# Kernel optimization log

Measured on AMD Instinct MI355X. Metric: run time of the kernel, lower is better.

The kernel has to match this reference:

```python
import jax, jax.numpy as jnp
import numpy as np
import math

RC = 5.0            # radial cutoff rc_rad
ZETA = [1, 2, 3, 4] # zeta list from configs['zeta']=4

def _angular_consts(z):
    # all (lx,ly,lz) with lx+ly+lz <= z (code generates n in range(z+1) and expands
    # each n into its non-negative integer triples)
    tri = []
    for lx in range(z + 1):
        for ly in range(z + 1 - lx):
            for lz in range(z + 1 - lx - ly):
                tri.append((lx, ly, lz))
    tri = np.array(tri, np.int32)
    n = tri.sum(1)
    # fact_norm = (n!/(lx!ly!lz!)) * (z!/((z-n)! n!)) = z! / ((z-n)! lx! ly! lz!)
    c = np.array([math.factorial(z) / (math.factorial(z - int(s)) * math.factorial(int(a)) * math.factorial(int(b)) * math.factorial(int(d)))
                  for (a, b, d), s in zip(tri, n)], np.float32)
    sign = ((-1.0) ** n).astype(np.float32)  # lambda=-1 channel: (1-cos)^z expansion
    return tri, c, sign

ANG = [_angular_consts(z) for z in ZETA]
silu = jax.nn.silu


def setup_inputs() -> dict:
    key = jax.random.key(0)
    ks = jax.random.split(key, 16)
    nat, npairs, Nrad, nzeta, emb, nelem = 2048, 65536, 8, 4, 4, 4
    feat = (Nrad + Nrad * 2 * nzeta) * emb  # 288
    L = 20.0
    pos = jax.random.uniform(ks[0], (nat, 3), jnp.float32) * L
    cell = L * jnp.eye(3, dtype=jnp.float32)
    i1 = jax.random.randint(ks[1], (npairs,), 0, nat, jnp.int32)
    i2 = jax.random.randint(ks[2], (npairs,), 0, nat, jnp.int32)
    shift = jnp.zeros((npairs, 3), jnp.int32)
    ids = jax.random.randint(ks[3], (nat,), 0, nelem, jnp.int32)
    onehot = jax.nn.one_hot(ids, nelem, dtype=jnp.float32)
    def W(k, i, o):
        return jax.random.normal(k, (i, o), jnp.float32) * 0.1
    return dict(
        positions=pos, cell=cell, species_onehot=onehot,
        sw1=W(ks[4], nelem, 64), sb1=jnp.zeros((64,), jnp.float32),
        sw2=W(ks[5], 64, emb), sb2=jnp.zeros((emb,), jnp.float32),
        rw1=W(ks[6], Nrad, 64), rb1=jnp.zeros((64,), jnp.float32),
        rw2=W(ks[7], 64, (nzeta + 1) * Nrad), rb2=jnp.zeros(((nzeta + 1) * Nrad,), jnp.float32),
        aw1=W(ks[8], feat, 256), ab1=jnp.zeros((256,), jnp.float32),
        aw2=W(ks[9], 256, 128), ab2=jnp.zeros((128,), jnp.float32),
        aw3=W(ks[10], 128, 1), ab3=jnp.zeros((1,), jnp.float32),
        first_atom_idx=i1, second_atom_idx=i2, shift_vectors=shift,
    )


def reference(positions, cell, species_onehot, sw1, sb1, sw2, sb2,
              rw1, rb1, rw2, rb2, aw1, ab1, aw2, ab2, aw3, ab3,
              first_atom_idx, second_atom_idx, shift_vectors):
    nat = positions.shape[0]
    Nrad = rw1.shape[0]
    nzeta = rw2.shape[1] // Nrad - 1
    # pair displacement vectors with PBC shifts
    rij = (positions[second_atom_idx] - positions[first_atom_idx]
           + shift_vectors.astype(jnp.float32) @ cell)            # [P,3]
    r = jnp.sqrt(jnp.sum(rij * rij, axis=-1) + 1e-12)             # [P]
    u = rij / r[:, None]                                          # unit vectors
    fc = jnp.where(r < RC, 0.5 * (jnp.cos(jnp.pi * r / RC) + 1.0), 0.0)
    # Gaussian radial basis -> learned radial functions (silu MLP, linear head)
    centers = jnp.linspace(0.0, RC, Nrad)
    w = RC / Nrad
    basis = jnp.exp(-((r[:, None] - centers) ** 2) / (2.0 * w * w)) * fc[:, None]
    rad = silu(basis @ rw1 + rb1) @ rw2 + rb2
    rad = rad.reshape(-1, nzeta + 1, Nrad) * fc[:, None, None]    # [P, nzeta+1, Nrad]
    # species encoder MLP -> per-atom embedding, gathered onto neighbor side
    semb = silu(species_onehot @ sw1 + sb1) @ sw2 + sb2           # [nat, emb]
    sp = semb[second_atom_idx]                                    # [P, emb]
    seg = lambda v: jax.ops.segment_sum(v, first_atom_idx, num_segments=nat)
    # two-body radial descriptor [nat, Nrad, emb]
    R = seg(rad[:, 0, :, None] * sp[:, None, :])
    feats = [R.reshape(nat, -1)]
    # three-body angular descriptors via multinomial (lx,ly,lz) expansion
    for zi in range(nzeta):
        tri, c, sign = ANG[zi]
        l = jnp.asarray(tri, jnp.float32)                         # [L,3]
        g = jnp.prod(u[:, None, :] ** l[None], axis=-1)           # [P,L] u^lx u^ly u^lz
        t = rad[:, 1 + zi, :, None, None] * g[:, None, :, None] * sp[:, None, None, :]
        G = seg(t)                                                # [nat,Nrad,L,emb]
        G2 = G * G
        Ap = jnp.einsum('inle,l->ine', G2, jnp.asarray(c))        # sum_jk f f (1+cos)^z
        Am = jnp.einsum('inle,l->ine', G2, jnp.asarray(c * sign)) # sum_jk f f (1-cos)^z
        feats += [Ap.reshape(nat, -1), Am.reshape(nat, -1)]
    F = jnp.concatenate(feats, axis=-1)                           # [nat, feature_size]
    h = silu(F @ aw1 + ab1)
    h = silu(h @ aw2 + ab2)
    e = h @ aw3 + ab3                                             # per-atom energies
    return jnp.sum(e)


if __name__ == '__main__':
    out = reference(**setup_inputs())
    print(out)
```

## Files before the change

### kernel.cpp

```cpp
#include <hip/hip_runtime.h>
#include <cmath>

#define NAT  2048
#define NP   65536
#define CAP  64
#define SCAP 8192
#define SSTR 120
#define PPB  256

__constant__ int GLX[70] = {0,
  0,0,0,1,
  0,0,0,0,0,0,1,1,1,2,
  0,0,0,0,0,0,0,0,0,0,1,1,1,1,1,1,2,2,2,3,
  0,0,0,0,0,0,0,0,0,0,0,0,0,0,0,1,1,1,1,1,1,1,1,1,1,2,2,2,2,2,2,3,3,3,4};
__constant__ int GLY[70] = {0,
  0,0,1,0,
  0,0,0,1,1,2,0,0,1,0,
  0,0,0,0,1,1,1,2,2,3,0,0,0,1,1,2,0,0,1,0,
  0,0,0,0,0,1,1,1,1,2,2,2,3,3,4,0,0,0,0,1,1,1,2,2,3,0,0,0,1,1,2,0,0,1,0};
__constant__ int GLZ[70] = {0,
  0,1,0,0,
  0,1,2,0,1,0,0,1,0,0,
  0,1,2,3,0,1,2,0,1,0,0,1,2,0,1,0,0,1,0,0,
  0,1,2,3,4,0,1,2,3,0,1,2,0,1,0,0,1,2,3,0,1,2,0,1,0,0,1,2,0,1,0,0,1,0,0};
__constant__ float C_ALL[69] = {
  1,1,1,1,
  1,2,1,2,2,1,2,2,2,1,
  1,3,3,1,3,6,3,3,3,1,3,6,3,6,6,3,3,3,3,1,
  1,4,6,4,1,4,12,12,4,6,12,6,4,4,1,4,12,12,4,12,24,12,12,12,4,6,12,6,12,12,6,4,4,4,1};
__constant__ float CS_ALL[69] = {
  1,-1,-1,-1,
  1,-2,1,-2,2,1,-2,2,2,1,
  1,-3,3,-1,-3,6,-3,3,-3,-1,-3,6,-3,6,-6,-3,3,-3,-3,-1,
  1,-4,6,-4,1,-4,12,-12,4,6,-12,6,-4,4,1,-4,12,-12,4,12,-24,12,-12,12,4,6,-12,6,-12,12,6,-4,4,4,1};
__constant__ int LTAB[4]    = {4,10,20,35};
__constant__ int CUMTAB[4]  = {0,4,14,34};
__constant__ int BASETAB[4] = {32,160,480,1120};

__device__ __forceinline__ float silu_f(float x){ return x / (1.0f + expf(-x)); }

__global__ void k_zero(int* __restrict__ p){
  const int idx = blockIdx.x*256 + threadIdx.x;
  if (idx < 2050) p[idx] = 0;
}

__global__ __launch_bounds__(256) void k_fstage(
    const float* __restrict__ pos, const float* __restrict__ cell,
    const float* __restrict__ oneh,
    const int* __restrict__ i1, const int* __restrict__ i2,
    const int* __restrict__ sv,
    const float* __restrict__ sw1, const float* __restrict__ sb1,
    const float* __restrict__ sw2, const float* __restrict__ sb2,
    const float* __restrict__ rw1, const float* __restrict__ rb1,
    const float* __restrict__ rw2, const float* __restrict__ rb2,
    int* __restrict__ cursor, int* __restrict__ nflat,
    int* __restrict__ ord_pid, int* __restrict__ ord_flat,
    float* __restrict__ staged)
{
  __shared__ float sembt[4][4];
  __shared__ int   spidL[PPB];
  __shared__ int   nsurvS, baseS;
  __shared__ float geo[8][5];
  __shared__ int   gspec[8];
  __shared__ float basis[8][8];
  __shared__ float hbuf[8][64];

  const int tid = threadIdx.x, lane = tid & 63, wid = tid >> 6;

  {
    float h = silu_f(sb1[lane] + sw1[wid*64 + lane]);
    const float4 w2 = ((const float4*)sw2)[lane];
    float q0=h*w2.x, q1=h*w2.y, q2=h*w2.z, q3=h*w2.w;
#pragma unroll
    for (int off=32; off>0; off>>=1){
      q0 += __shfl_xor(q0, off); q1 += __shfl_xor(q1, off);
      q2 += __shfl_xor(q2, off); q3 += __shfl_xor(q3, off);
    }
    if (lane < 4){
      float v = (lane==0) ? q0+sb2[0] : (lane==1) ? q1+sb2[1]
              : (lane==2) ? q2+sb2[2] : q3+sb2[3];
      sembt[wid][lane] = v;
    }
  }
  if (tid == 0) nsurvS = 0;
  __syncthreads();

  {
    const int p = blockIdx.x*PPB + tid;
    const int a = i1[p], b = i2[p];
    const float s0=(float)sv[p*3+0], s1=(float)sv[p*3+1], s2=(float)sv[p*3+2];
    const float rx = pos[b*3+0]-pos[a*3+0] + s0*cell[0]+s1*cell[3]+s2*cell[6];
    const float ry = pos[b*3+1]-pos[a*3+1] + s0*cell[1]+s1*cell[4]+s2*cell[7];
    const float rz = pos[b*3+2]-pos[a*3+2] + s0*cell[2]+s1*cell[5]+s2*cell[8];
    const float r = sqrtf(rx*rx+ry*ry+rz*rz + 1e-12f);
    if (r < 5.0f){
      int ls = atomicAdd(&nsurvS, 1);
      spidL[ls] = p;
    }
  }
  __syncthreads();
  const int ns = nsurvS;
  if (ns == 0) return;
  if (tid == 0) baseS = atomicAdd(nflat, ns);
  __syncthreads();
  const int fbase = baseS;

  if (tid < ns){
    const int p = spidL[tid];
    const int a = i1[p];
    const int fs = fbase + tid;
    int s = atomicAdd(&cursor[a], 1);
    if (s < CAP){ ord_pid[a*CAP+s] = p; ord_flat[a*CAP+s] = fs; }
  }
  __syncthreads();

  for (int j0=0; j0<ns; j0+=8){
    const int nj = (ns-j0 < 8) ? (ns-j0) : 8;
    if (tid < nj){
      const int p = spidL[j0+tid];
      const int a = i1[p], b = i2[p];
      const float s0=(float)sv[p*3+0], s1=(float)sv[p*3+1], s2=(float)sv[p*3+2];
      const float rx = pos[b*3+0]-pos[a*3+0] + s0*cell[0]+s1*cell[3]+s2*cell[6];
      const float ry = pos[b*3+1]-pos[a*3+1] + s0*cell[1]+s1*cell[4]+s2*cell[7];
      const float rz = pos[b*3+2]-pos[a*3+2] + s0*cell[2]+s1*cell[5]+s2*cell[8];
      const float r  = sqrtf(rx*rx+ry*ry+rz*rz + 1e-12f);
      const float inv= 1.0f/r;
      geo[tid][0]=r; geo[tid][1]=rx*inv; geo[tid][2]=ry*inv; geo[tid][3]=rz*inv;
      geo[tid][4]=0.5f*(cosf(0.6283185307179586f*r)+1.0f);
      const float o1=oneh[b*4+1], o2=oneh[b*4+2], o3=oneh[b*4+3];
      gspec[tid] = (int)(o1 + 2.0f*o2 + 3.0f*o3 + 0.5f);
    }
    __syncthreads();
    if (tid < nj*8){
      const int j=tid>>3, k=tid&7;
      const float d = geo[j][0] - (float)k*(5.0f/7.0f);
      basis[j][k] = expf(-d*d*1.28f)*geo[j][4];
    }
    __syncthreads();
    for (int idx=tid; idx<nj*64; idx+=256){
      const int j=idx>>6, o=idx&63;
      float h = rb1[o];
#pragma unroll
      for (int k=0;k<8;k++) h += basis[j][k]*rw1[k*64+o];
      hbuf[j][o] = silu_f(h);
    }
    __syncthreads();
    for (int idx=tid; idx<nj*40; idx+=256){
      const int j=idx/40, n=idx-j*40;
      float racc = rb2[n];
#pragma unroll 8
      for (int o=0;o<64;o++) racc += hbuf[j][o]*rw2[o*40+n];
      const int fs = fbase + j0 + j;
      if (fs < SCAP) staged[(size_t)fs*SSTR + n] = racc*geo[j][4];
    }
    for (int idx=tid; idx<nj*70; idx+=256){
      const int j=idx/70, l=idx-j*70;
      const float ux=geo[j][1], uy=geo[j][2], uz=geo[j][3];
      const int ex=GLX[l], ey=GLY[l], ez=GLZ[l];
      float g=1.f;
      for (int q=0;q<ex;q++) g*=ux;
      for (int q=0;q<ey;q++) g*=uy;
      for (int q=0;q<ez;q++) g*=uz;
      const int fs = fbase + j0 + j;
      if (fs < SCAP) staged[(size_t)fs*SSTR + 40 + l] = g;
    }
    if (tid < nj*4){
      const int j=tid>>2, e=tid&3;
      const int fs = fbase + j0 + j;
      if (fs < SCAP) staged[(size_t)fs*SSTR + 110 + e] = sembt[gspec[j]][e];
    }
    __syncthreads();
  }
}

__global__ __launch_bounds__(256) void k_feat(
    const int* __restrict__ cursor,
    const int* __restrict__ ord_pid, const int* __restrict__ ord_flat,
    const float* __restrict__ staged, float* __restrict__ Fout)
{
  const int atom = blockIdx.x, tid = threadIdx.x;
  __shared__ float G[2240];
  __shared__ float sdata[8][SSTR];
  __shared__ int opid[CAP];
  __shared__ int pslot[CAP];
  __shared__ int sflb[8];

  int cnt = cursor[atom]; if (cnt > CAP) cnt = CAP;
  if (tid < CAP) opid[tid] = (tid < cnt) ? ord_pid[atom*CAP + tid] : 0x7fffffff;
  __syncthreads();
  if (tid < cnt){
    int my = opid[tid]; int rk = 0;
    for (int j=0;j<cnt;j++) rk += (opid[j] < my);
    pslot[rk] = tid;
  }

  float acc[9];
  int ridx[9], gidx[9], eidx[9];
#pragma unroll
  for (int k=0;k<9;k++){
    acc[k]=0.f;
    int a = tid + (k<<8);
    int ri=0, gi=0, ei=0;
    if (a < 32){ ri = a>>2; gi = 0; ei = a&3; }
    else if (a < 2240){
      int b = a-32; int lb, nl, l, n;
      if (b < 128)      { lb=b;      ei=lb&3; nl=lb>>2; l=nl%4;  n=nl/4;  ri=8 +n; gi=1 +l; }
      else if (b < 448) { lb=b-128;  ei=lb&3; nl=lb>>2; l=nl%10; n=nl/10; ri=16+n; gi=5 +l; }
      else if (b < 1088){ lb=b-448;  ei=lb&3; nl=lb>>2; l=nl%20; n=nl/20; ri=24+n; gi=15+l; }
      else              { lb=b-1088; ei=lb&3; nl=lb>>2; l=nl%35; n=nl/35; ri=32+n; gi=35+l; }
    }
    ridx[k]=ri; gidx[k]=gi; eidx[k]=ei;
  }
  __syncthreads();

  for (int c0=0; c0<cnt; c0+=8){
    const int nc = (cnt-c0 < 8) ? (cnt-c0) : 8;
    if (tid < nc) sflb[tid] = ord_flat[atom*CAP + pslot[c0+tid]];
    __syncthreads();
    for (int idx=tid; idx<nc*SSTR; idx+=256){
      int jj = idx/SSTR, i = idx - jj*SSTR;
      int fsl = sflb[jj];
      sdata[jj][i] = (fsl < SCAP) ? staged[(size_t)fsl*SSTR + i] : 0.f;
    }
    __syncthreads();
    for (int jj=0;jj<nc;jj++){
      const float* sd = sdata[jj];
#pragma unroll
      for (int k=0;k<9;k++)
        acc[k] += sd[ridx[k]] * sd[40+gidx[k]] * sd[110+eidx[k]];
    }
    __syncthreads();
  }

#pragma unroll
  for (int k=0;k<9;k++){
    int a = tid + (k<<8);
    if (a < 2240) G[a] = acc[k];
  }
  __syncthreads();

  float* Fo = Fout + atom*288;
  if (tid < 32) Fo[tid] = G[tid];
  if (tid < 128){
    const int zi = tid>>5, n=(tid>>2)&7, e=tid&3;
    const int L = LTAB[zi], cb = CUMTAB[zi], bs = BASETAB[zi];
    float ap=0.f, am=0.f;
    for (int l=0;l<L;l++){
      float v  = G[bs + ((n*L + l)<<2) + e];
      float v2 = v*v;
      ap += C_ALL [cb+l]*v2;
      am += CS_ALL[cb+l]*v2;
    }
    Fo[32 + (zi<<6)      + (n<<2) + e] = ap;
    Fo[32 + (zi<<6) + 32 + (n<<2) + e] = am;
  }
}

__global__ __launch_bounds__(256) void k_mlpreg(
    const float* __restrict__ F,
    const float* __restrict__ aw1, const float* __restrict__ ab1,
    const float* __restrict__ aw2, const float* __restrict__ ab2,
    const float* __restrict__ aw3, const float* __restrict__ ab3,
    float* __restrict__ partials, int* __restrict__ done,
    float* __restrict__ out)
{
  __shared__ float Hs[8][256];
  __shared__ float es[8];
  __shared__ int   winner;
  const int tid = threadIdx.x;
  const int abase = blockIdx.x*8;

  {
    const int c = tid;
    float acc[8];
#pragma unroll
    for (int a=0;a<8;a++) acc[a]=0.f;
    const float* Fb = F + (size_t)abase*288;
    for (int i=0;i<288;i++){
      const float w = aw1[(size_t)i*256 + c];
#pragma unroll
      for (int a=0;a<8;a++)
        acc[a] += Fb[a*288 + i] * w;
    }
    const float b = ab1[c];
#pragma unroll
    for (int a=0;a<8;a++) Hs[a][c] = silu_f(acc[a] + b);
  }
  __syncthreads();

  {
    const int c2 = tid & 127, h = tid >> 7;
    float acc2[4] = {0.f,0.f,0.f,0.f};
    for (int i4=0; i4<256; i4+=4){
      const float w0 = aw2[(size_t)(i4+0)*128 + c2];
      const float w1 = aw2[(size_t)(i4+1)*128 + c2];
      const float w2 = aw2[(size_t)(i4+2)*128 + c2];
      const float w3 = aw2[(size_t)(i4+3)*128 + c2];
#pragma unroll
      for (int q=0;q<4;q++){
        const float4 h4 = *(const float4*)&Hs[h*4+q][i4];
        acc2[q] += h4.x*w0 + h4.y*w1 + h4.z*w2 + h4.w*w3;
      }
    }
    const float b  = ab2[c2];
    const float w3h = aw3[c2];
    float p = silu_f(acc2[0]+b)*w3h;
    float p1 = silu_f(acc2[1]+b)*w3h;
    float p2 = silu_f(acc2[2]+b)*w3h;
    float p3 = silu_f(acc2[3]+b)*w3h;
    __shared__ float part[4][4][2];
    const int wv = tid >> 6, lane = tid & 63;
    float s0=p, s1=p1, s2=p2, s3=p3;
#pragma unroll
    for (int off=32; off>0; off>>=1){
      s0 += __shfl_xor(s0, off); s1 += __shfl_xor(s1, off);
      s2 += __shfl_xor(s2, off); s3 += __shfl_xor(s3, off);
    }
    if (lane == 0){
      part[wv][0][0]=s0; part[wv][1][0]=s1; part[wv][2][0]=s2; part[wv][3][0]=s3;
    }
    __syncthreads();
    if (tid < 8){
      const int hh = tid >> 2, q = tid & 3;
      es[hh*4+q] = part[2*hh][q][0] + part[2*hh+1][q][0];
    }
  }
  __syncthreads();
  if (tid == 0){
    float bsum = es[0]+es[1]+es[2]+es[3]+es[4]+es[5]+es[6]+es[7] + 8.0f*ab3[0];
    __hip_atomic_store(&partials[blockIdx.x], bsum,
                       __ATOMIC_RELEASE, __HIP_MEMORY_SCOPE_AGENT);
    int old = __hip_atomic_fetch_add(done, 1, __ATOMIC_ACQ_REL,
                                     __HIP_MEMORY_SCOPE_AGENT);
    winner = (old == (NAT/8) - 1) ? 1 : 0;
  }
  __syncthreads();

  if (winner && tid < 64){
    float s = 0.f;
#pragma unroll
    for (int q=0;q<4;q++)
      s += __hip_atomic_load(&partials[tid*4+q],
                             __ATOMIC_ACQUIRE, __HIP_MEMORY_SCOPE_AGENT);
    for (int off=32; off>0; off>>=1) s += __shfl_xor(s, off);
    if (tid == 0) out[0] = s;
  }
}

extern "C" void kernel_launch(void* const* d_in, const int* in_sizes, int n_in,
                              void* d_out, int out_size, void* d_ws, size_t ws_size,
                              hipStream_t stream) {
  const float* pos  = (const float*)d_in[0];
  const float* cell = (const float*)d_in[1];
  const float* oneh = (const float*)d_in[2];
  const float* sw1  = (const float*)d_in[3];
  const float* sb1  = (const float*)d_in[4];
  const float* sw2  = (const float*)d_in[5];
  const float* sb2  = (const float*)d_in[6];
  const float* rw1  = (const float*)d_in[7];
  const float* rb1  = (const float*)d_in[8];
  const float* rw2  = (const float*)d_in[9];
  const float* rb2  = (const float*)d_in[10];
  const float* aw1  = (const float*)d_in[11];
  const float* ab1  = (const float*)d_in[12];
  const float* aw2  = (const float*)d_in[13];
  const float* ab2  = (const float*)d_in[14];
  const float* aw3  = (const float*)d_in[15];
  const float* ab3  = (const float*)d_in[16];
  const int*   i1   = (const int*)d_in[17];
  const int*   i2   = (const int*)d_in[18];
  const int*   sv   = (const int*)d_in[19];

  char* ws = (char*)d_ws;
  int*   cursor   = (int*)  (ws + 0);
  int*   nflat    = (int*)  (ws + 8192);
  int*   done     = (int*)  (ws + 8196);
  int*   ord_pid  = (int*)  (ws + 8448);
  int*   ord_flat = (int*)  (ws + 532736);
  float* staged   = (float*)(ws + 1057024);
  float* F        = (float*)(ws + 4989184);
  float* partials = (float*)(ws + 7348480);

  k_zero  <<<9,       256, 0, stream>>>(cursor);
  k_fstage<<<NP/PPB,  256, 0, stream>>>(pos, cell, oneh, i1, i2, sv,
                                        sw1, sb1, sw2, sb2,
                                        rw1, rb1, rw2, rb2,
                                        cursor, nflat, ord_pid, ord_flat, staged);
  k_feat  <<<NAT,     256, 0, stream>>>(cursor, ord_pid, ord_flat, staged, F);
  k_mlpreg<<<NAT/8,   256, 0, stream>>>(F, aw1, ab1, aw2, ab2, aw3, ab3,
                                        partials, done, (float*)d_out);
}
```

Measured before the change: 77.83 us.

## Split MLP reduction across 1024 threads and vectorize staged row gather

The MLP kernel now runs 1024 threads per block. The first layer's 288-long input dimension is split into four slices whose partial sums go to shared memory and are reduced there, and the second layer gives each thread one atom instead of four. This is meant to raise parallelism in the latency-bound MLP, which has only 256 blocks, at the cost of extra shared memory and a barrier. Separately, the per-pair staged row copy in k_feat now uses float4 loads, cutting the number of load instructions.

```diff
diff --git a/kernel.cpp b/kernel.cpp
--- a/kernel.cpp
+++ b/kernel.cpp
@@ -180,7 +180,7 @@
 {
   const int atom = blockIdx.x, tid = threadIdx.x;
   __shared__ float G[2240];
-  __shared__ float sdata[8][SSTR];
+  __shared__ __align__(16) float sdata[8][SSTR];
   __shared__ int opid[CAP];
   __shared__ int pslot[CAP];
   __shared__ int sflb[8];
@@ -217,10 +217,12 @@
     const int nc = (cnt-c0 < 8) ? (cnt-c0) : 8;
     if (tid < nc) sflb[tid] = ord_flat[atom*CAP + pslot[c0+tid]];
     __syncthreads();
-    for (int idx=tid; idx<nc*SSTR; idx+=256){
-      int jj = idx/SSTR, i = idx - jj*SSTR;
+    for (int idx=tid; idx<nc*30; idx+=256){
+      int jj = idx/30, q = idx - jj*30;
       int fsl = sflb[jj];
-      sdata[jj][i] = (fsl < SCAP) ? staged[(size_t)fsl*SSTR + i] : 0.f;
+      float4 v = make_float4(0.f,0.f,0.f,0.f);
+      if (fsl < SCAP) v = ((const float4*)(staged + (size_t)fsl*SSTR))[q];
+      ((float4*)sdata[jj])[q] = v;
     }
     __syncthreads();
     for (int jj=0;jj<nc;jj++){
@@ -256,7 +258,7 @@
   }
 }
 
-__global__ __launch_bounds__(256) void k_mlpreg(
+__global__ __launch_bounds__(1024) void k_mlp4(
     const float* __restrict__ F,
     const float* __restrict__ aw1, const float* __restrict__ ab1,
     const float* __restrict__ aw2, const float* __restrict__ ab2,
@@ -264,67 +266,63 @@
     float* __restrict__ partials, int* __restrict__ done,
     float* __restrict__ out)
 {
+  __shared__ float P1s[4][8][256];
   __shared__ float Hs[8][256];
+  __shared__ float part[16];
   __shared__ float es[8];
   __shared__ int   winner;
   const int tid = threadIdx.x;
   const int abase = blockIdx.x*8;
+  const float* Fb = F + (size_t)abase*288;
 
   {
-    const int c = tid;
+    const int q = tid >> 8, c = tid & 255;
+    const int i0 = q*72;
     float acc[8];
 #pragma unroll
     for (int a=0;a<8;a++) acc[a]=0.f;
-    const float* Fb = F + (size_t)abase*288;
-    for (int i=0;i<288;i++){
-      const float w = aw1[(size_t)i*256 + c];
+    for (int ib=0; ib<18; ++ib){
+      const int i = i0 + ib*4;
+      float4 f4[8];
+#pragma unroll
+      for (int a=0;a<8;a++) f4[a] = *(const float4*)&Fb[a*288 + i];
+      const float w0 = aw1[(size_t)(i+0)*256 + c];
+      const float w1 = aw1[(size_t)(i+1)*256 + c];
+      const float w2 = aw1[(size_t)(i+2)*256 + c];
+      const float w3 = aw1[(size_t)(i+3)*256 + c];
 #pragma unroll
       for (int a=0;a<8;a++)
-        acc[a] += Fb[a*288 + i] * w;
-    }
-    const float b = ab1[c];
-#pragma unroll
-    for (int a=0;a<8;a++) Hs[a][c] = silu_f(acc[a] + b);
+        acc[a] += f4[a].x*w0 + f4[a].y*w1 + f4[a].z*w2 + f4[a].w*w3;
+    }
+#pragma unroll
+    for (int a=0;a<8;a++) P1s[q][a][c] = acc[a];
+  }
+  __syncthreads();
+
+  for (int idx = tid; idx < 2048; idx += 1024){
+    const int a = idx >> 8, c = idx & 255;
+    Hs[a][c] = silu_f(ab1[c] + P1s[0][a][c] + P1s[1][a][c]
+                              + P1s[2][a][c] + P1s[3][a][c]);
   }
   __syncthreads();
 
   {
-    const int c2 = tid & 127, h = tid >> 7;
-    float acc2[4] = {0.f,0.f,0.f,0.f};
-    for (int i4=0; i4<256; i4+=4){
-      const float w0 = aw2[(size_t)(i4+0)*128 + c2];
-      const float w1 = aw2[(size_t)(i4+1)*128 + c2];
-      const float w2 = aw2[(size_t)(i4+2)*128 + c2];
-      const float w3 = aw2[(size_t)(i4+3)*128 + c2];
-#pragma unroll
-      for (int q=0;q<4;q++){
-        const float4 h4 = *(const float4*)&Hs[h*4+q][i4];
-        acc2[q] += h4.x*w0 + h4.y*w1 + h4.z*w2 + h4.w*w3;
-      }
-    }
-    const float b  = ab2[c2];
-    const float w3h = aw3[c2];
-    float p = silu_f(acc2[0]+b)*w3h;
-    float p1 = silu_f(acc2[1]+b)*w3h;
-    float p2 = silu_f(acc2[2]+b)*w3h;
-    float p3 = silu_f(acc2[3]+b)*w3h;
-    __shared__ float part[4][4][2];
+    const int a = tid >> 7, c2 = tid & 127;
+    float acc2 = 0.f;
+    for (int ib=0; ib<64; ++ib){
+      const int i = ib*4;
+      const float4 h4 = *(const float4*)&Hs[a][i];
+      acc2 += h4.x*aw2[(size_t)(i+0)*128 + c2] + h4.y*aw2[(size_t)(i+1)*128 + c2]
+            + h4.z*aw2[(size_t)(i+2)*128 + c2] + h4.w*aw2[(size_t)(i+3)*128 + c2];
+    }
+    float p = silu_f(acc2 + ab2[c2]) * aw3[c2];
     const int wv = tid >> 6, lane = tid & 63;
-    float s0=p, s1=p1, s2=p2, s3=p3;
-#pragma unroll
-    for (int off=32; off>0; off>>=1){
-      s0 += __shfl_xor(s0, off); s1 += __shfl_xor(s1, off);
-      s2 += __shfl_xor(s2, off); s3 += __shfl_xor(s3, off);
-    }
-    if (lane == 0){
-      part[wv][0][0]=s0; part[wv][1][0]=s1; part[wv][2][0]=s2; part[wv][3][0]=s3;
-    }
-    __syncthreads();
-    if (tid < 8){
-      const int hh = tid >> 2, q = tid & 3;
-      es[hh*4+q] = part[2*hh][q][0] + part[2*hh+1][q][0];
-    }
-  }
+#pragma unroll
+    for (int off=32; off>0; off>>=1) p += __shfl_xor(p, off);
+    if (lane == 0) part[wv] = p;
+  }
+  __syncthreads();
+  if (tid < 8) es[tid] = part[2*tid] + part[2*tid+1];
   __syncthreads();
   if (tid == 0){
     float bsum = es[0]+es[1]+es[2]+es[3]+es[4]+es[5]+es[6]+es[7] + 8.0f*ab3[0];
@@ -387,6 +385,6 @@
                                         rw1, rb1, rw2, rb2,
                                         cursor, nflat, ord_pid, ord_flat, staged);
   k_feat  <<<NAT,     256, 0, stream>>>(cursor, ord_pid, ord_flat, staged, F);
-  k_mlpreg<<<NAT/8,   256, 0, stream>>>(F, aw1, ab1, aw2, ab2, aw3, ab3,
+  k_mlp4  <<<NAT/8,  1024, 0, stream>>>(F, aw1, ab1, aw2, ab2, aw3, ab3,
                                         partials, done, (float*)d_out);
 }
```

Result: slower. 82.49 us (+6.0%).
